# Kernel optimization log

Measured on AMD Instinct MI355X. Metric: run time of the kernel, lower is better.

## Reference

```python
import jax, jax.numpy as jnp
import numpy as np

DIM = 512
NUM_HEADS = 8
HEAD_DIM = DIM // NUM_HEADS
SCALE = HEAD_DIM ** -0.5


def setup_inputs() -> dict:
    key = jax.random.key(0)
    ks = jax.random.split(key, 10)
    B, Sq, Skv = 4, 2048, 2048
    std = DIM ** -0.5
    return {
        "x1": jax.random.normal(ks[0], (B, Sq, DIM), jnp.float32),
        "x2": jax.random.normal(ks[1], (B, Skv, DIM), jnp.float32),
        "Wq": jax.random.normal(ks[2], (DIM, DIM), jnp.float32) * std,
        "bq": jax.random.normal(ks[3], (DIM,), jnp.float32) * 0.02,
        "Wk": jax.random.normal(ks[4], (DIM, DIM), jnp.float32) * std,
        "bk": jax.random.normal(ks[5], (DIM,), jnp.float32) * 0.02,
        "Wv": jax.random.normal(ks[6], (DIM, DIM), jnp.float32) * std,
        "bv": jax.random.normal(ks[7], (DIM,), jnp.float32) * 0.02,
        "Wo": jax.random.normal(ks[8], (DIM, DIM), jnp.float32) * std,
        "bo": jax.random.normal(ks[9], (DIM,), jnp.float32) * 0.02,
    }


def reference(x1, x2, Wq, bq, Wk, bk, Wv, bv, Wo, bo):
    B, Sq, _ = x1.shape
    Skv = x2.shape[1]
    # Linear projections (torch nn.Linear: x @ W.T + b)
    Q = (x1 @ Wq.T + bq).reshape(B, Sq, NUM_HEADS, HEAD_DIM)
    K = (x2 @ Wk.T + bk).reshape(B, Skv, NUM_HEADS, HEAD_DIM)
    V = (x2 @ Wv.T + bv).reshape(B, Skv, NUM_HEADS, HEAD_DIM)
    # [B, H, Sq, Skv]
    attn = jnp.einsum("bqhd,bkhd->bhqk", Q, K) * SCALE
    attn = jax.nn.softmax(attn, axis=-1)  # dropout is identity in eval mode
    out = jnp.einsum("bhqk,bkhd->bqhd", attn, V).reshape(B, Sq, DIM)
    return out @ Wo.T + bo
```

## Files before the change

kernel.cpp:

```cpp
#include <hip/hip_runtime.h>
#include <math.h>

constexpr int kB = 4, kS = 2048, kDim = 512, kNH = 8, kHD = 64;
constexpr float kQScale = 0.18033688011112042f;

using bf16x8 = __attribute__((ext_vector_type(8))) short;
using f32x4  = __attribute__((ext_vector_type(4))) float;

__device__ __forceinline__ unsigned pack_rn(float f0, float f1) {
  unsigned a = __builtin_bit_cast(unsigned, f0) + 0x8000u;
  unsigned b = __builtin_bit_cast(unsigned, f1) + 0x8000u;
  return __builtin_amdgcn_perm(b, a, 0x07060302u);
}
__device__ __forceinline__ float fexp2(float x) {
#if __has_builtin(__builtin_amdgcn_exp2f)
  return __builtin_amdgcn_exp2f(x);
#else
  return exp2f(x);
#endif
}

#define GLDS(gp, lp) __builtin_amdgcn_global_load_lds(                         \
    (const __attribute__((address_space(1))) void*)(gp),                       \
    (__attribute__((address_space(3))) void*)(lp), 16, 0, 0)

__global__ __launch_bounds__(256) void cvt_bf16(
    const float* __restrict__ x1, const float* __restrict__ x2,
    const float* __restrict__ Wq, const float* __restrict__ Wk,
    const float* __restrict__ Wv, const float* __restrict__ Wo,
    unsigned short* __restrict__ x1b, unsigned short* __restrict__ x2b,
    unsigned short* __restrict__ wb) {
  const size_t i = (size_t)blockIdx.x * 256 + threadIdx.x;
  const float* src;
  unsigned short* dst;
  size_t off;
  if (i < 1048576) { src = x1; dst = x1b; off = i; }
  else if (i < 2097152) { src = x2; dst = x2b; off = i - 1048576; }
  else {
    const size_t j = i - 2097152;
    const int seg = (int)(j >> 16);
    src = seg == 0 ? Wq : seg == 1 ? Wk : seg == 2 ? Wv : Wo;
    dst = wb + (size_t)seg * 262144;
    off = j & 65535;
  }
  const float4 v = *(const float4*)(src + off * 4);
  uint2 o;
  o.x = pack_rn(v.x, v.y);
  o.y = pack_rn(v.z, v.w);
  *(uint2*)(dst + off * 4) = o;
}

__global__ __launch_bounds__(256, 2) void qkv_gemm(
    const unsigned short* __restrict__ x1b, const unsigned short* __restrict__ x2b,
    const unsigned short* __restrict__ wb,
    const float* __restrict__ bq, const float* __restrict__ bk,
    const float* __restrict__ bv,
    unsigned short* __restrict__ Qg, unsigned short* __restrict__ Kg,
    unsigned short* __restrict__ Vg) {
  __shared__ __align__(16) short As[2][128 * 64];
  __shared__ __align__(16) short Bs[2][128 * 64];
  const int z = blockIdx.z;
  const unsigned short* X = z ? x2b : x1b;
  const unsigned short* W = wb + (size_t)z * (kDim * kDim);
  const float* bias = (z == 0) ? bq : (z == 1) ? bk : bv;

  const int t = threadIdx.x, lane = t & 63, w = t >> 6;
  const int g = lane >> 4, c = lane & 15;
  const int bm = blockIdx.y * 128, bn = blockIdx.x * 128;
  const int wm = (w >> 1) * 64, wn = (w & 1) * 64;

  const int srow = lane >> 3;
  const int schunk = ((lane & 7) ^ srow) * 8;
  const int wrow = w * 32;

#pragma unroll
  for (int i8 = 0; i8 < 4; ++i8) {
    const int row = wrow + i8 * 8;
    GLDS(X + (size_t)(bm + row + srow) * kDim + schunk, &As[0][row * 64]);
    GLDS(W + (size_t)(bn + row + srow) * kDim + schunk, &Bs[0][row * 64]);
  }
  __syncthreads();

  f32x4 acc[16] = {};
  int ib = 0;
  for (int k0 = 0; k0 < kDim; k0 += 64, ib ^= 1) {
    if (k0 + 64 < kDim) {
      const int nb = ib ^ 1;
#pragma unroll
      for (int i8 = 0; i8 < 4; ++i8) {
        const int row = wrow + i8 * 8;
        GLDS(X + (size_t)(bm + row + srow) * kDim + k0 + 64 + schunk, &As[nb][row * 64]);
        GLDS(W + (size_t)(bn + row + srow) * kDim + k0 + 64 + schunk, &Bs[nb][row * 64]);
      }
    }
#pragma unroll
    for (int kk = 0; kk < 2; ++kk) {
      const int sx = ((kk * 4 + g) ^ (c & 7)) * 8;
      if (z == 2) {
        bf16x8 fa[4], fb[4];
#pragma unroll
        for (int i = 0; i < 4; ++i) fa[i] = *(const bf16x8*)&As[ib][(wm + i * 16 + c) * 64 + sx];
#pragma unroll
        for (int j = 0; j < 4; ++j) fb[j] = *(const bf16x8*)&Bs[ib][(wn + j * 16 + c) * 64 + sx];
#pragma unroll
        for (int i = 0; i < 4; ++i)
#pragma unroll
          for (int j = 0; j < 4; ++j)
            acc[i * 4 + j] = __builtin_amdgcn_mfma_f32_16x16x32_bf16(fa[i], fb[j], acc[i * 4 + j], 0, 0, 0);
      } else {
        bf16x8 fa[4], fb[4];
#pragma unroll
        for (int i = 0; i < 4; ++i) fa[i] = *(const bf16x8*)&Bs[ib][(wn + i * 16 + c) * 64 + sx];
#pragma unroll
        for (int j = 0; j < 4; ++j) fb[j] = *(const bf16x8*)&As[ib][(wm + j * 16 + c) * 64 + sx];
#pragma unroll
        for (int i = 0; i < 4; ++i)
#pragma unroll
          for (int j = 0; j < 4; ++j)
            acc[i * 4 + j] = __builtin_amdgcn_mfma_f32_16x16x32_bf16(fa[i], fb[j], acc[i * 4 + j], 0, 0, 0);
      }
    }
    __syncthreads();
  }

  if (z == 2) {
    const int h_ = (bn + wn) >> 6;
#pragma unroll
    for (int i = 0; i < 4; ++i)
#pragma unroll
      for (int j = 0; j < 4; ++j) {
        const int n = bn + wn + j * 16 + c;
        const float bb = bias[n];
        const int m0 = bm + wm + i * 16 + g * 4;
        const int b_ = m0 >> 11, s0 = m0 & 2047;
        const int d_ = n & 63;
        const f32x4 a = acc[i * 4 + j];
        uint2 pv;
        pv.x = pack_rn(a[0] + bb, a[1] + bb);
        pv.y = pack_rn(a[2] + bb, a[3] + bb);
        *(uint2*)(Vg + (((size_t)((b_ * kNH + h_) * kHD + d_)) << 11) + s0) = pv;
      }
  } else {
    const float sc = (z == 0) ? kQScale : 1.0f;
    unsigned short* Og = z ? Kg : Qg;
    const int h_ = (bn + wn) >> 6;
#pragma unroll
    for (int i = 0; i < 4; ++i) {
      const int n0 = bn + wn + i * 16 + g * 4;
      const float4 bb = *(const float4*)(bias + n0);
      const int d0 = n0 & 63;
#pragma unroll
      for (int j = 0; j < 4; ++j) {
        const int m = bm + wm + j * 16 + c;
        const int b_ = m >> 11, s_ = m & 2047;
        const f32x4 a = acc[i * 4 + j];
        uint2 st;
        st.x = pack_rn((a[0] + bb.x) * sc, (a[1] + bb.y) * sc);
        st.y = pack_rn((a[2] + bb.z) * sc, (a[3] + bb.w) * sc);
        *(uint2*)(Og + (((size_t)((b_ * kNH + h_) * kS + s_)) << 6) + d0) = st;
      }
    }
  }
}

__global__ __launch_bounds__(256, 2) void out_gemm(const unsigned short* __restrict__ A,
                                                   const unsigned short* __restrict__ Wob,
                                                   const float* __restrict__ bias,
                                                   float* __restrict__ Y) {
  __shared__ __align__(16) short As[2][128 * 64];
  __shared__ __align__(16) short Bs[2][128 * 64];
  const int t = threadIdx.x, lane = t & 63, w = t >> 6;
  const int g = lane >> 4, c = lane & 15;
  const int bm = blockIdx.y * 128, bn = blockIdx.x * 128;
  const int wm = (w >> 1) * 64, wn = (w & 1) * 64;
  const int srow = lane >> 3;
  const int schunk = ((lane & 7) ^ srow) * 8;
  const int wrow = w * 32;

#pragma unroll
  for (int i8 = 0; i8 < 4; ++i8) {
    const int row = wrow + i8 * 8;
    GLDS(A + (size_t)(bm + row + srow) * kDim + schunk, &As[0][row * 64]);
    GLDS(Wob + (size_t)(bn + row + srow) * kDim + schunk, &Bs[0][row * 64]);
  }
  __syncthreads();

  f32x4 acc[16] = {};
  int ib = 0;
  for (int k0 = 0; k0 < kDim; k0 += 64, ib ^= 1) {
    if (k0 + 64 < kDim) {
      const int nb = ib ^ 1;
#pragma unroll
      for (int i8 = 0; i8 < 4; ++i8) {
        const int row = wrow + i8 * 8;
        GLDS(A + (size_t)(bm + row + srow) * kDim + k0 + 64 + schunk, &As[nb][row * 64]);
        GLDS(Wob + (size_t)(bn + row + srow) * kDim + k0 + 64 + schunk, &Bs[nb][row * 64]);
      }
    }
#pragma unroll
    for (int kk = 0; kk < 2; ++kk) {
      const int sx = ((kk * 4 + g) ^ (c & 7)) * 8;
      bf16x8 fa[4], fb[4];
#pragma unroll
      for (int i = 0; i < 4; ++i) fa[i] = *(const bf16x8*)&Bs[ib][(wn + i * 16 + c) * 64 + sx];
#pragma unroll
      for (int j = 0; j < 4; ++j) fb[j] = *(const bf16x8*)&As[ib][(wm + j * 16 + c) * 64 + sx];
#pragma unroll
      for (int i = 0; i < 4; ++i)
#pragma unroll
        for (int j = 0; j < 4; ++j)
          acc[i * 4 + j] = __builtin_amdgcn_mfma_f32_16x16x32_bf16(fa[i], fb[j], acc[i * 4 + j], 0, 0, 0);
    }
    __syncthreads();
  }
#pragma unroll
  for (int i = 0; i < 4; ++i) {
    const int n0 = bn + wn + i * 16 + g * 4;
    const float4 bb = *(const float4*)(bias + n0);
#pragma unroll
    for (int j = 0; j < 4; ++j) {
      const int m = bm + wm + j * 16 + c;
      const f32x4 a = acc[i * 4 + j];
      float4 st;
      st.x = a[0] + bb.x;
      st.y = a[1] + bb.y;
      st.z = a[2] + bb.z;
      st.w = a[3] + bb.w;
      *(float4*)(Y + (size_t)m * kDim + n0) = st;
    }
  }
}

__global__ __launch_bounds__(512, 4) void flash_mfma(const unsigned short* __restrict__ Qg,
                                                     const unsigned short* __restrict__ Kg,
                                                     const unsigned short* __restrict__ Vg,
                                                     unsigned short* __restrict__ attn) {
  __shared__ __align__(16) short Ks[64 * 76];
  __shared__ __align__(16) short Vs[64 * 76];
  const int t = threadIdx.x, lane = t & 63, w = t >> 6;
  const int c = lane & 15, g4 = lane >> 4;
  const int bh = blockIdx.x, q0 = blockIdx.y * 256;
  const int b_ = bh >> 3, h_ = bh & 7;

  const unsigned short* Qp = Qg + ((size_t)bh * kS + q0) * kHD;
  const unsigned short* Kp = Kg + (size_t)bh * kS * kHD;
  const unsigned short* Vp = Vg + (size_t)bh * kHD * kS;

  bf16x8 bq[2][2];
  {
    const unsigned short* qr = Qp + (size_t)(w * 32 + c) * kHD + g4 * 8;
    bq[0][0] = *(const bf16x8*)qr;
    bq[1][0] = *(const bf16x8*)(qr + 32);
    bq[0][1] = *(const bf16x8*)(qr + 16 * kHD);
    bq[1][1] = *(const bf16x8*)(qr + 16 * kHD + 32);
  }

  const int r0 = t >> 3, cc0 = (t & 7) * 8;
  const int ps = (r0 & 32) | (((r0 >> 2) & 1) << 4) | (((r0 >> 3) & 3) << 2) | (r0 & 3);
  const unsigned short* kpt = Kp + (size_t)r0 * kHD + cc0;
  const unsigned short* vpt = Vp + (size_t)r0 * kS + cc0;
  uint4 pk0 = *(const uint4*)kpt;
  uint4 pv0 = *(const uint4*)vpt;
  kpt += 64 * kHD;
  vpt += 64;

  float l[2] = {0.f, 0.f};
  f32x4 o[4][2] = {};

  for (int kv0 = 0; kv0 < kS; kv0 += 64) {
    __syncthreads();
    *(uint4*)&Ks[ps * 76 + cc0] = pk0;
    *(uint4*)&Vs[r0 * 76 + cc0] = pv0;
    __syncthreads();
    if (kv0 + 64 < kS) {
      pk0 = *(const uint4*)kpt;
      pv0 = *(const uint4*)vpt;
      kpt += 64 * kHD;
      vpt += 64;
    }

    f32x4 sa[4][2] = {};
#pragma unroll
    for (int ks = 0; ks < 2; ++ks)
#pragma unroll
      for (int kt = 0; kt < 4; ++kt) {
        const bf16x8 a = *(const bf16x8*)&Ks[(kt * 16 + c) * 76 + ks * 32 + g4 * 8];
        sa[kt][0] = __builtin_amdgcn_mfma_f32_16x16x32_bf16(a, bq[ks][0], sa[kt][0], 0, 0, 0);
        sa[kt][1] = __builtin_amdgcn_mfma_f32_16x16x32_bf16(a, bq[ks][1], sa[kt][1], 0, 0, 0);
      }

#pragma unroll
    for (int ks = 0; ks < 2; ++ks) {
      bf16x8 bpf[2];
#pragma unroll
      for (int qs = 0; qs < 2; ++qs) {
        const float p0 = fexp2(sa[2 * ks][qs][0]), p1 = fexp2(sa[2 * ks][qs][1]);
        const float p2 = fexp2(sa[2 * ks][qs][2]), p3 = fexp2(sa[2 * ks][qs][3]);
        const float p4 = fexp2(sa[2 * ks + 1][qs][0]), p5 = fexp2(sa[2 * ks + 1][qs][1]);
        const float p6 = fexp2(sa[2 * ks + 1][qs][2]), p7 = fexp2(sa[2 * ks + 1][qs][3]);
        l[qs] += ((p0 + p1) + (p2 + p3)) + ((p4 + p5) + (p6 + p7));
        uint4 bp;
        bp.x = pack_rn(p0, p1);
        bp.y = pack_rn(p2, p3);
        bp.z = pack_rn(p4, p5);
        bp.w = pack_rn(p6, p7);
        bpf[qs] = __builtin_bit_cast(bf16x8, bp);
      }
#pragma unroll
      for (int dt = 0; dt < 4; ++dt) {
        const bf16x8 va = *(const bf16x8*)&Vs[(dt * 16 + c) * 76 + ks * 32 + g4 * 8];
        o[dt][0] = __builtin_amdgcn_mfma_f32_16x16x32_bf16(va, bpf[0], o[dt][0], 0, 0, 0);
        o[dt][1] = __builtin_amdgcn_mfma_f32_16x16x32_bf16(va, bpf[1], o[dt][1], 0, 0, 0);
      }
    }
  }

#pragma unroll
  for (int qs = 0; qs < 2; ++qs) {
    l[qs] += __shfl_xor(l[qs], 16, 64);
    l[qs] += __shfl_xor(l[qs], 32, 64);
  }
#pragma unroll
  for (int qs = 0; qs < 2; ++qs) {
    const float inv = 1.0f / l[qs];
    unsigned short* orow =
        attn + ((size_t)(b_ * kS + q0 + w * 32 + qs * 16 + c)) * kDim + h_ * kHD;
#pragma unroll
    for (int dt = 0; dt < 4; ++dt) {
      uint2 st;
      st.x = pack_rn(o[dt][qs][0] * inv, o[dt][qs][1] * inv);
      st.y = pack_rn(o[dt][qs][2] * inv, o[dt][qs][3] * inv);
      *(uint2*)(orow + dt * 16 + g4 * 4) = st;
    }
  }
}

extern "C" void kernel_launch(void* const* d_in, const int* in_sizes, int n_in,
                              void* d_out, int out_size, void* d_ws, size_t ws_size,
                              hipStream_t stream) {
  const float* x1 = (const float*)d_in[0];
  const float* x2 = (const float*)d_in[1];
  const float* Wq = (const float*)d_in[2];
  const float* bq = (const float*)d_in[3];
  const float* Wk = (const float*)d_in[4];
  const float* bk = (const float*)d_in[5];
  const float* Wv = (const float*)d_in[6];
  const float* bv = (const float*)d_in[7];
  const float* Wo = (const float*)d_in[8];
  const float* bo = (const float*)d_in[9];
  float* out = (float*)d_out;

  constexpr size_t kTok = (size_t)kB * kS * kDim;
  unsigned short* x1b = (unsigned short*)d_ws;
  unsigned short* x2b = x1b + kTok;
  unsigned short* wb  = x2b + kTok;
  unsigned short* Qg  = wb + 4 * (size_t)(kDim * kDim);
  unsigned short* Kg  = Qg + kTok;
  unsigned short* Vg  = Kg + kTok;
  unsigned short* atb = Vg + kTok;

  const dim3 blk(256);
  cvt_bf16<<<dim3(9216), blk, 0, stream>>>(x1, x2, Wq, Wk, Wv, Wo, x1b, x2b, wb);
  qkv_gemm<<<dim3(4, 64, 3), blk, 0, stream>>>(x1b, x2b, wb, bq, bk, bv, Qg, Kg, Vg);
  flash_mfma<<<dim3(32, 8), dim3(512), 0, stream>>>(Qg, Kg, Vg, atb);
  out_gemm<<<dim3(4, 64), blk, 0, stream>>>(atb, wb + 3 * (size_t)(kDim * kDim), bo, out);
}
```

Measured before the change: 181.0 us.

## Split KV range across two wave halves in flash attention with LDS reduction

Each block now covers 128 query rows instead of 256. Its 8 waves form two groups of 4, and each group processes alternate 64-key chunks from a 128-key staging tile. The partial outputs and row sums from the second group are summed into the first group through shared memory before normalisation. This doubles the grid from 256 to 512 blocks, giving more parallelism on the many-CU device, at the cost of twice the LDS, an extra reduction step, and K/V being loaded once per 128 queries instead of once per 256.

```diff
diff --git a/kernel.cpp b/kernel.cpp
--- a/kernel.cpp
+++ b/kernel.cpp
@@ -235,11 +235,15 @@
                                                      const unsigned short* __restrict__ Kg,
                                                      const unsigned short* __restrict__ Vg,
                                                      unsigned short* __restrict__ attn) {
-  __shared__ __align__(16) short Ks[64 * 76];
-  __shared__ __align__(16) short Vs[64 * 76];
+  __shared__ __align__(16) short SMEM[2 * 2 * 64 * 76];
+  short* Ksm = SMEM;
+  short* Vsm = SMEM + 2 * 64 * 76;
+
   const int t = threadIdx.x, lane = t & 63, w = t >> 6;
+  const int wq = w & 3;
+  const int half = w >> 2;
   const int c = lane & 15, g4 = lane >> 4;
-  const int bh = blockIdx.x, q0 = blockIdx.y * 256;
+  const int bh = blockIdx.x, q0 = blockIdx.y * 128;
   const int b_ = bh >> 3, h_ = bh & 7;
 
   const unsigned short* Qp = Qg + ((size_t)bh * kS + q0) * kHD;
@@ -248,7 +252,7 @@
 
   bf16x8 bq[2][2];
   {
-    const unsigned short* qr = Qp + (size_t)(w * 32 + c) * kHD + g4 * 8;
+    const unsigned short* qr = Qp + (size_t)(wq * 32 + c) * kHD + g4 * 8;
     bq[0][0] = *(const bf16x8*)qr;
     bq[1][0] = *(const bf16x8*)(qr + 32);
     bq[0][1] = *(const bf16x8*)(qr + 16 * kHD);
@@ -260,23 +264,32 @@
   const unsigned short* kpt = Kp + (size_t)r0 * kHD + cc0;
   const unsigned short* vpt = Vp + (size_t)r0 * kS + cc0;
   uint4 pk0 = *(const uint4*)kpt;
+  uint4 pk1 = *(const uint4*)(kpt + 64 * kHD);
   uint4 pv0 = *(const uint4*)vpt;
-  kpt += 64 * kHD;
-  vpt += 64;
+  uint4 pv1 = *(const uint4*)(vpt + 64);
+  kpt += 128 * kHD;
+  vpt += 128;
+
+  const short* Kb = Ksm + half * (64 * 76);
+  const short* Vb = Vsm + half * (64 * 76);
 
   float l[2] = {0.f, 0.f};
   f32x4 o[4][2] = {};
 
-  for (int kv0 = 0; kv0 < kS; kv0 += 64) {
+  for (int kvb = 0; kvb < kS; kvb += 128) {
     __syncthreads();
-    *(uint4*)&Ks[ps * 76 + cc0] = pk0;
-    *(uint4*)&Vs[r0 * 76 + cc0] = pv0;
+    *(uint4*)&Ksm[ps * 76 + cc0] = pk0;
+    *(uint4*)&Ksm[64 * 76 + ps * 76 + cc0] = pk1;
+    *(uint4*)&Vsm[r0 * 76 + cc0] = pv0;
+    *(uint4*)&Vsm[64 * 76 + r0 * 76 + cc0] = pv1;
     __syncthreads();
-    if (kv0 + 64 < kS) {
+    if (kvb + 128 < kS) {
       pk0 = *(const uint4*)kpt;
+      pk1 = *(const uint4*)(kpt + 64 * kHD);
       pv0 = *(const uint4*)vpt;
-      kpt += 64 * kHD;
-      vpt += 64;
+      pv1 = *(const uint4*)(vpt + 64);
+      kpt += 128 * kHD;
+      vpt += 128;
     }
 
     f32x4 sa[4][2] = {};
@@ -284,7 +297,7 @@
     for (int ks = 0; ks < 2; ++ks)
 #pragma unroll
       for (int kt = 0; kt < 4; ++kt) {
-        const bf16x8 a = *(const bf16x8*)&Ks[(kt * 16 + c) * 76 + ks * 32 + g4 * 8];
+        const bf16x8 a = *(const bf16x8*)&Kb[(kt * 16 + c) * 76 + ks * 32 + g4 * 8];
         sa[kt][0] = __builtin_amdgcn_mfma_f32_16x16x32_bf16(a, bq[ks][0], sa[kt][0], 0, 0, 0);
         sa[kt][1] = __builtin_amdgcn_mfma_f32_16x16x32_bf16(a, bq[ks][1], sa[kt][1], 0, 0, 0);
       }
@@ -308,29 +321,55 @@
       }
 #pragma unroll
       for (int dt = 0; dt < 4; ++dt) {
-        const bf16x8 va = *(const bf16x8*)&Vs[(dt * 16 + c) * 76 + ks * 32 + g4 * 8];
+        const bf16x8 va = *(const bf16x8*)&Vb[(dt * 16 + c) * 76 + ks * 32 + g4 * 8];
         o[dt][0] = __builtin_amdgcn_mfma_f32_16x16x32_bf16(va, bpf[0], o[dt][0], 0, 0, 0);
         o[dt][1] = __builtin_amdgcn_mfma_f32_16x16x32_bf16(va, bpf[1], o[dt][1], 0, 0, 0);
       }
     }
   }
 
-#pragma unroll
-  for (int qs = 0; qs < 2; ++qs) {
-    l[qs] += __shfl_xor(l[qs], 16, 64);
-    l[qs] += __shfl_xor(l[qs], 32, 64);
-  }
-#pragma unroll
-  for (int qs = 0; qs < 2; ++qs) {
-    const float inv = 1.0f / l[qs];
-    unsigned short* orow =
-        attn + ((size_t)(b_ * kS + q0 + w * 32 + qs * 16 + c)) * kDim + h_ * kHD;
-#pragma unroll
-    for (int dt = 0; dt < 4; ++dt) {
-      uint2 st;
-      st.x = pack_rn(o[dt][qs][0] * inv, o[dt][qs][1] * inv);
-      st.y = pack_rn(o[dt][qs][2] * inv, o[dt][qs][3] * inv);
-      *(uint2*)(orow + dt * 16 + g4 * 4) = st;
+  float* ex = (float*)SMEM;
+  __syncthreads();
+  if (half == 1) {
+    float* eo = ex + (wq * 64 + lane) * 32;
+#pragma unroll
+    for (int dt = 0; dt < 4; ++dt)
+#pragma unroll
+      for (int qs = 0; qs < 2; ++qs)
+#pragma unroll
+        for (int r = 0; r < 4; ++r) eo[dt * 8 + qs * 4 + r] = o[dt][qs][r];
+    ex[8192 + (wq * 64 + lane) * 2 + 0] = l[0];
+    ex[8192 + (wq * 64 + lane) * 2 + 1] = l[1];
+  }
+  __syncthreads();
+  if (half == 0) {
+    const float* eo = ex + (wq * 64 + lane) * 32;
+#pragma unroll
+    for (int dt = 0; dt < 4; ++dt)
+#pragma unroll
+      for (int qs = 0; qs < 2; ++qs)
+#pragma unroll
+        for (int r = 0; r < 4; ++r) o[dt][qs][r] += eo[dt * 8 + qs * 4 + r];
+    l[0] += ex[8192 + (wq * 64 + lane) * 2 + 0];
+    l[1] += ex[8192 + (wq * 64 + lane) * 2 + 1];
+
+#pragma unroll
+    for (int qs = 0; qs < 2; ++qs) {
+      l[qs] += __shfl_xor(l[qs], 16, 64);
+      l[qs] += __shfl_xor(l[qs], 32, 64);
+    }
+#pragma unroll
+    for (int qs = 0; qs < 2; ++qs) {
+      const float inv = 1.0f / l[qs];
+      unsigned short* orow =
+          attn + ((size_t)(b_ * kS + q0 + wq * 32 + qs * 16 + c)) * kDim + h_ * kHD;
+#pragma unroll
+      for (int dt = 0; dt < 4; ++dt) {
+        uint2 st;
+        st.x = pack_rn(o[dt][qs][0] * inv, o[dt][qs][1] * inv);
+        st.y = pack_rn(o[dt][qs][2] * inv, o[dt][qs][3] * inv);
+        *(uint2*)(orow + dt * 16 + g4 * 4) = st;
+      }
     }
   }
 }
@@ -362,6 +401,6 @@
   const dim3 blk(256);
   cvt_bf16<<<dim3(9216), blk, 0, stream>>>(x1, x2, Wq, Wk, Wv, Wo, x1b, x2b, wb);
   qkv_gemm<<<dim3(4, 64, 3), blk, 0, stream>>>(x1b, x2b, wb, bq, bk, bv, Qg, Kg, Vg);
-  flash_mfma<<<dim3(32, 8), dim3(512), 0, stream>>>(Qg, Kg, Vg, atb);
+  flash_mfma<<<dim3(32, 16), dim3(512), 0, stream>>>(Qg, Kg, Vg, atb);
   out_gemm<<<dim3(4, 64), blk, 0, stream>>>(atb, wb + 3 * (size_t)(kDim * kDim), bo, out);
 }
```

After: 271.6 us. 50.1% more time.
